# Kernel optimization log

Hardware: AMD Instinct MI355X
Metric: run time of the kernel (lower is better)

The kernel has to match this reference:

```python
import jax, jax.numpy as jnp
import numpy as np


def setup_inputs() -> dict:
    key = jax.random.key(0)
    x = jax.random.uniform(key, (64_000_000,), dtype=jnp.float32)
    return {"x": x, "bins": 100}


def reference(x, bins):
    # torch.histc semantics with min=max=0.0: use data min/max as the range.
    xf = x.reshape(-1)
    hmin = jnp.min(xf)
    hmax = jnp.max(xf)
    # guard degenerate range (torch widens it; with random data this is a no-op)
    hmax = jnp.where(hmax == hmin, hmin + 1.0, hmax)
    scale = bins / (hmax - hmin)
    # bin index: floor((x - min) * bins / (max - min)); value == max lands in last bin
    idx = jnp.clip(jnp.floor((xf - hmin) * scale).astype(jnp.int32), 0, bins - 1)
    in_range = (xf >= hmin) & (xf <= hmax)  # out-of-range elements are ignored
    weights = in_range.astype(xf.dtype)
    hist = jax.ops.segment_sum(weights, idx, num_segments=bins)
    return hist
```

## Files before the change

kernel.cpp:

```cpp
#include <hip/hip_runtime.h>

#define NBLOCKS   2048
#define NTHREADS  256
#define UNROLL    8

__global__ __launch_bounds__(NTHREADS)
void minmax_partial(const float4* __restrict__ x4, long n4,
                    const float* __restrict__ xtail, long ntail,
                    float* __restrict__ pmin, float* __restrict__ pmax) {
    __shared__ float smin[NTHREADS / 64], smax[NTHREADS / 64];
    const long tid = blockIdx.x * (long)blockDim.x + threadIdx.x;
    const long nth = (long)gridDim.x * blockDim.x;

    float m0 = INFINITY, M0 = -INFINITY, m1 = INFINITY, M1 = -INFINITY;

    const long chunk = nth * UNROLL;
    const long limit = (n4 / chunk) * chunk;
    for (long j = tid; j < limit; j += chunk) {
        float4 v[UNROLL];
        #pragma unroll
        for (int u = 0; u < UNROLL; ++u) v[u] = x4[j + (long)u * nth];
        #pragma unroll
        for (int u = 0; u < UNROLL; u += 2) {
            m0 = fminf(m0, fminf(fminf(v[u].x, v[u].y), fminf(v[u].z, v[u].w)));
            M0 = fmaxf(M0, fmaxf(fmaxf(v[u].x, v[u].y), fmaxf(v[u].z, v[u].w)));
            m1 = fminf(m1, fminf(fminf(v[u+1].x, v[u+1].y), fminf(v[u+1].z, v[u+1].w)));
            M1 = fmaxf(M1, fmaxf(fmaxf(v[u+1].x, v[u+1].y), fmaxf(v[u+1].z, v[u+1].w)));
        }
    }
    for (long j = limit + tid; j < n4; j += nth) {
        float4 v = x4[j];
        m0 = fminf(m0, fminf(fminf(v.x, v.y), fminf(v.z, v.w)));
        M0 = fmaxf(M0, fmaxf(fmaxf(v.x, v.y), fmaxf(v.z, v.w)));
    }
    for (long j = tid; j < ntail; j += nth) {
        float v = xtail[j];
        m0 = fminf(m0, v);
        M0 = fmaxf(M0, v);
    }

    float lm = fminf(m0, m1), lM = fmaxf(M0, M1);
    for (int off = 32; off; off >>= 1) {
        lm = fminf(lm, __shfl_xor(lm, off));
        lM = fmaxf(lM, __shfl_xor(lM, off));
    }
    if ((threadIdx.x & 63) == 0) {
        smin[threadIdx.x >> 6] = lm;
        smax[threadIdx.x >> 6] = lM;
    }
    __syncthreads();
    if (threadIdx.x == 0) {
        float bm = smin[0], bM = smax[0];
        for (int w = 1; w < NTHREADS / 64; ++w) { bm = fminf(bm, smin[w]); bM = fmaxf(bM, smax[w]); }
        pmin[blockIdx.x] = bm;
        pmax[blockIdx.x] = bM;
    }
}

__global__ void reduce_minmax(const float* __restrict__ pmin, const float* __restrict__ pmax,
                              int nblocks, float* __restrict__ mm,
                              float* __restrict__ out, int bins) {
    __shared__ float smin[NTHREADS / 64], smax[NTHREADS / 64];
    float lm = INFINITY, lM = -INFINITY;
    for (int i = threadIdx.x; i < nblocks; i += blockDim.x) {
        lm = fminf(lm, pmin[i]);
        lM = fmaxf(lM, pmax[i]);
    }
    for (int off = 32; off; off >>= 1) {
        lm = fminf(lm, __shfl_xor(lm, off));
        lM = fmaxf(lM, __shfl_xor(lM, off));
    }
    if ((threadIdx.x & 63) == 0) {
        smin[threadIdx.x >> 6] = lm;
        smax[threadIdx.x >> 6] = lM;
    }
    __syncthreads();
    if (threadIdx.x == 0) {
        float bm = smin[0], bM = smax[0];
        for (int w = 1; w < NTHREADS / 64; ++w) { bm = fminf(bm, smin[w]); bM = fmaxf(bM, smax[w]); }
        mm[0] = bm;
        mm[1] = bM;
    }
    for (int b = threadIdx.x; b < bins; b += blockDim.x) out[b] = 0.0f;
}

__global__ __launch_bounds__(NTHREADS)
void hist_kernel(const float4* __restrict__ x4, long n4,
                 const float* __restrict__ xtail, long ntail,
                 const float* __restrict__ mm,
                 float* __restrict__ out, int bins) {
    extern __shared__ unsigned sh[];
    const int nw = NTHREADS / 64;
    unsigned* h = sh + (threadIdx.x >> 6) * bins;

    for (int b = threadIdx.x; b < nw * bins; b += blockDim.x) sh[b] = 0u;
    __syncthreads();

    const float hmin = mm[0];
    float hmax = mm[1];
    if (hmax == hmin) hmax = hmin + 1.0f;
    const float scale = (float)bins / (hmax - hmin);
    const int bmax = bins - 1;

    const long tid = blockIdx.x * (long)blockDim.x + threadIdx.x;
    const long nth = (long)gridDim.x * blockDim.x;
    const long chunk = nth * UNROLL;
    const long limit = (n4 / chunk) * chunk;

    for (long j = tid; j < limit; j += chunk) {
        float4 v[UNROLL];
        #pragma unroll
        for (int u = 0; u < UNROLL; ++u) v[u] = x4[j + (long)u * nth];
        #pragma unroll
        for (int u = 0; u < UNROLL; ++u) {
            int b0 = min(max((int)((v[u].x - hmin) * scale), 0), bmax);
            int b1 = min(max((int)((v[u].y - hmin) * scale), 0), bmax);
            int b2 = min(max((int)((v[u].z - hmin) * scale), 0), bmax);
            int b3 = min(max((int)((v[u].w - hmin) * scale), 0), bmax);
            atomicAdd(&h[b0], 1u);
            atomicAdd(&h[b1], 1u);
            atomicAdd(&h[b2], 1u);
            atomicAdd(&h[b3], 1u);
        }
    }
    for (long j = limit + tid; j < n4; j += nth) {
        float4 v = x4[j];
        int b0 = min(max((int)((v.x - hmin) * scale), 0), bmax);
        int b1 = min(max((int)((v.y - hmin) * scale), 0), bmax);
        int b2 = min(max((int)((v.z - hmin) * scale), 0), bmax);
        int b3 = min(max((int)((v.w - hmin) * scale), 0), bmax);
        atomicAdd(&h[b0], 1u);
        atomicAdd(&h[b1], 1u);
        atomicAdd(&h[b2], 1u);
        atomicAdd(&h[b3], 1u);
    }
    for (long j = tid; j < ntail; j += nth) {
        int b0 = min(max((int)((xtail[j] - hmin) * scale), 0), bmax);
        atomicAdd(&h[b0], 1u);
    }
    __syncthreads();

    for (int b = threadIdx.x; b < bins; b += blockDim.x) {
        unsigned t = 0;
        for (int w = 0; w < nw; ++w) t += sh[w * bins + b];
        if (t) atomicAdd(&out[b], (float)t);
    }
}

extern "C" void kernel_launch(void* const* d_in, const int* in_sizes, int n_in,
                              void* d_out, int out_size, void* d_ws, size_t ws_size,
                              hipStream_t stream) {
    const float* x = (const float*)d_in[0];
    long n = (long)in_sizes[0];
    int bins = out_size;

    long n4 = n >> 2;
    long ntail = n - (n4 << 2);
    const float4* x4 = (const float4*)x;
    const float* xtail = x + (n4 << 2);

    float* out = (float*)d_out;
    float* ws = (float*)d_ws;
    float* pmin = ws;
    float* pmax = ws + NBLOCKS;
    float* mm   = ws + 2 * NBLOCKS;

    const size_t shbytes = (size_t)(NTHREADS / 64) * bins * sizeof(unsigned);

    minmax_partial<<<NBLOCKS, NTHREADS, 0, stream>>>(x4, n4, xtail, ntail, pmin, pmax);
    reduce_minmax<<<1, NTHREADS, 0, stream>>>(pmin, pmax, NBLOCKS, mm, out, bins);
    hist_kernel<<<NBLOCKS, NTHREADS, shbytes, stream>>>(x4, n4, xtail, ntail, mm, out, bins);
}
```

Baseline: 428.8 us.

## Reverse minmax traversal, add per-half-wave histogram copies, halve grid

The min/max pass now walks chunks from the end of the array backward, so it starts on data most recently touched by the forward histogram pass and may still find it in the large last-level cache. The histogram uses one shared-memory copy per 32 threads instead of per 64-thread wave, reducing LDS atomic contention at the cost of more shared memory. The grid is halved, occupancy hints are added to launch bounds, and min/max uses four independent accumulators.

```diff
diff --git a/kernel.cpp b/kernel.cpp
--- a/kernel.cpp
+++ b/kernel.cpp
@@ -1,10 +1,11 @@
 #include <hip/hip_runtime.h>
 
-#define NBLOCKS   2048
+#define NBLOCKS   1024
 #define NTHREADS  256
 #define UNROLL    8
+#define NCOPIES   (NTHREADS / 32)
 
-__global__ __launch_bounds__(NTHREADS)
+__global__ __launch_bounds__(NTHREADS, 4)
 void minmax_partial(const float4* __restrict__ x4, long n4,
                     const float* __restrict__ xtail, long ntail,
                     float* __restrict__ pmin, float* __restrict__ pmax) {
@@ -13,22 +14,29 @@
     const long nth = (long)gridDim.x * blockDim.x;
 
     float m0 = INFINITY, M0 = -INFINITY, m1 = INFINITY, M1 = -INFINITY;
+    float m2 = INFINITY, M2 = -INFINITY, m3 = INFINITY, M3 = -INFINITY;
 
-    const long chunk = nth * UNROLL;
-    const long limit = (n4 / chunk) * chunk;
-    for (long j = tid; j < limit; j += chunk) {
+    const long chunk   = nth * UNROLL;
+    const long nchunks = n4 / chunk;
+
+    for (long c = nchunks; c-- > 0;) {
+        const long j = c * chunk + tid;
         float4 v[UNROLL];
         #pragma unroll
         for (int u = 0; u < UNROLL; ++u) v[u] = x4[j + (long)u * nth];
         #pragma unroll
-        for (int u = 0; u < UNROLL; u += 2) {
+        for (int u = 0; u < UNROLL; u += 4) {
             m0 = fminf(m0, fminf(fminf(v[u].x, v[u].y), fminf(v[u].z, v[u].w)));
             M0 = fmaxf(M0, fmaxf(fmaxf(v[u].x, v[u].y), fmaxf(v[u].z, v[u].w)));
             m1 = fminf(m1, fminf(fminf(v[u+1].x, v[u+1].y), fminf(v[u+1].z, v[u+1].w)));
             M1 = fmaxf(M1, fmaxf(fmaxf(v[u+1].x, v[u+1].y), fmaxf(v[u+1].z, v[u+1].w)));
+            m2 = fminf(m2, fminf(fminf(v[u+2].x, v[u+2].y), fminf(v[u+2].z, v[u+2].w)));
+            M2 = fmaxf(M2, fmaxf(fmaxf(v[u+2].x, v[u+2].y), fmaxf(v[u+2].z, v[u+2].w)));
+            m3 = fminf(m3, fminf(fminf(v[u+3].x, v[u+3].y), fminf(v[u+3].z, v[u+3].w)));
+            M3 = fmaxf(M3, fmaxf(fmaxf(v[u+3].x, v[u+3].y), fmaxf(v[u+3].z, v[u+3].w)));
         }
     }
-    for (long j = limit + tid; j < n4; j += nth) {
+    for (long j = nchunks * chunk + tid; j < n4; j += nth) {
         float4 v = x4[j];
         m0 = fminf(m0, fminf(fminf(v.x, v.y), fminf(v.z, v.w)));
         M0 = fmaxf(M0, fmaxf(fmaxf(v.x, v.y), fmaxf(v.z, v.w)));
@@ -39,7 +47,8 @@
         M0 = fmaxf(M0, v);
     }
 
-    float lm = fminf(m0, m1), lM = fmaxf(M0, M1);
+    float lm = fminf(fminf(m0, m1), fminf(m2, m3));
+    float lM = fmaxf(fmaxf(M0, M1), fmaxf(M2, M3));
     for (int off = 32; off; off >>= 1) {
         lm = fminf(lm, __shfl_xor(lm, off));
         lM = fmaxf(lM, __shfl_xor(lM, off));
@@ -84,16 +93,15 @@
     for (int b = threadIdx.x; b < bins; b += blockDim.x) out[b] = 0.0f;
 }
 
-__global__ __launch_bounds__(NTHREADS)
+__global__ __launch_bounds__(NTHREADS, 4)
 void hist_kernel(const float4* __restrict__ x4, long n4,
                  const float* __restrict__ xtail, long ntail,
                  const float* __restrict__ mm,
                  float* __restrict__ out, int bins) {
     extern __shared__ unsigned sh[];
-    const int nw = NTHREADS / 64;
-    unsigned* h = sh + (threadIdx.x >> 6) * bins;
+    unsigned* h = sh + (threadIdx.x >> 5) * bins;
 
-    for (int b = threadIdx.x; b < nw * bins; b += blockDim.x) sh[b] = 0u;
+    for (int b = threadIdx.x; b < NCOPIES * bins; b += blockDim.x) sh[b] = 0u;
     __syncthreads();
 
     const float hmin = mm[0];
@@ -104,10 +112,11 @@
 
     const long tid = blockIdx.x * (long)blockDim.x + threadIdx.x;
     const long nth = (long)gridDim.x * blockDim.x;
-    const long chunk = nth * UNROLL;
-    const long limit = (n4 / chunk) * chunk;
+    const long chunk   = nth * UNROLL;
+    const long nchunks = n4 / chunk;
 
-    for (long j = tid; j < limit; j += chunk) {
+    for (long c = 0; c < nchunks; ++c) {
+        const long j = c * chunk + tid;
         float4 v[UNROLL];
         #pragma unroll
         for (int u = 0; u < UNROLL; ++u) v[u] = x4[j + (long)u * nth];
@@ -123,7 +132,7 @@
             atomicAdd(&h[b3], 1u);
         }
     }
-    for (long j = limit + tid; j < n4; j += nth) {
+    for (long j = nchunks * chunk + tid; j < n4; j += nth) {
         float4 v = x4[j];
         int b0 = min(max((int)((v.x - hmin) * scale), 0), bmax);
         int b1 = min(max((int)((v.y - hmin) * scale), 0), bmax);
@@ -142,7 +151,8 @@
 
     for (int b = threadIdx.x; b < bins; b += blockDim.x) {
         unsigned t = 0;
-        for (int w = 0; w < nw; ++w) t += sh[w * bins + b];
+        #pragma unroll
+        for (int w = 0; w < NCOPIES; ++w) t += sh[w * bins + b];
         if (t) atomicAdd(&out[b], (float)t);
     }
 }
@@ -165,7 +175,7 @@
     float* pmax = ws + NBLOCKS;
     float* mm   = ws + 2 * NBLOCKS;
 
-    const size_t shbytes = (size_t)(NTHREADS / 64) * bins * sizeof(unsigned);
+    const size_t shbytes = (size_t)NCOPIES * bins * sizeof(unsigned);
 
     minmax_partial<<<NBLOCKS, NTHREADS, 0, stream>>>(x4, n4, xtail, ntail, pmin, pmax);
     reduce_minmax<<<1, NTHREADS, 0, stream>>>(pmin, pmax, NBLOCKS, mm, out, bins);
```

Result: faster. 402.7 us (-6.1%).
